# Optimization experiments

Hardware: AMD Instinct MI355X
Metric: run time of the kernel (lower is better)

## Reference

```python
import jax, jax.numpy as jnp
import numpy as np

MAX_N_LATENT = 8
EOS_THRESHOLD = 0.7
EOS_PATTERN_LEN = 3
COS_SIM_THRESHOLD = 0.3
EOS_SOFT_THRESHOLD = 0.5
CONTEXT_WINDOW = 2
EPS = 1e-8


def setup_inputs() -> dict:
    key = jax.random.key(0)
    k = jax.random.split(key, 8)
    B, S, D = 8, 4096, 1024
    s = 0.02
    latent_states = jax.random.normal(k[0], (B, S, D), dtype=jnp.float32)
    binary_mask = jax.random.randint(k[1], (B, S, 1), 0, 2).astype(jnp.int32)
    proj_w = jax.random.normal(k[2], (D, D), dtype=jnp.float32) * s
    proj_b = jax.random.normal(k[3], (D,), dtype=jnp.float32) * s
    eos_w1 = jax.random.normal(k[4], (D, D // 2), dtype=jnp.float32) * s
    eos_b1 = jax.random.normal(k[5], (D // 2,), dtype=jnp.float32) * s
    eos_w2 = jax.random.normal(k[6], (D // 2, 1), dtype=jnp.float32) * s
    eos_b2 = jax.random.normal(k[7], (1,), dtype=jnp.float32) * s
    return {"latent_states": latent_states, "binary_mask": binary_mask,
            "proj_w": proj_w, "proj_b": proj_b,
            "eos_w1": eos_w1, "eos_b1": eos_b1,
            "eos_w2": eos_w2, "eos_b2": eos_b2}


def reference(latent_states, binary_mask, proj_w, proj_b, eos_w1, eos_b1, eos_w2, eos_b2):
    B, S, D = latent_states.shape

    # ---- EOS scores (computed under no_grad in the original) ----
    h = jax.nn.relu(jnp.einsum('bsd,df->bsf', latent_states, eos_w1) + eos_b1)
    eos_scores = jax.nn.sigmoid(jnp.einsum('bsf,fo->bso', h, eos_w2) + eos_b2)[..., 0]
    eos_scores = jax.lax.stop_gradient(eos_scores)  # [B, S]

    # ---- segment ids: a boundary (mask==1) at i closes the patch that includes i ----
    m = binary_mask[..., 0].astype(jnp.int32)                 # [B, S]
    seg = jnp.cumsum(m, axis=1) - m                           # exclusive cumsum => patch id per token
    valid = (seg < MAX_N_LATENT).astype(latent_states.dtype)  # drop patches beyond MAX_N_LATENT (p[:max_patches])
    onehot = jax.nn.one_hot(jnp.clip(seg, 0, MAX_N_LATENT - 1), MAX_N_LATENT,
                            dtype=latent_states.dtype) * valid[..., None]  # [B, S, P]
    sums = jnp.einsum('bsp,bsd->bpd', onehot, latent_states)  # segmented sum
    counts = onehot.sum(axis=1)                               # [B, P]
    pooled = sums / jnp.maximum(counts, 1.0)[..., None]       # mean pooling; empty patches -> 0 (proj adds bias, as in torch)
    patches = jnp.einsum('bpd,do->bpo', pooled, proj_w) + proj_b  # [B, MAX_N_LATENT, output_dim]

    # ---- EOS bounds ----
    mthr = eos_scores > EOS_THRESHOLD
    run = mthr
    for t in range(1, EOS_PATTERN_LEN):                       # consecutive_eos_count >= EOS_PATTERN_LEN
        run = run & jnp.pad(mthr[:, :-t], ((0, 0), (t, 0)))
    a = latent_states[:, 1:-1]                                # prev state at i-1, for i >= 2
    b = latent_states[:, 2:]                                  # current state at i
    cos = (a * b).sum(-1) / (jnp.maximum(jnp.linalg.norm(a, axis=-1), EPS)
                             * jnp.maximum(jnp.linalg.norm(b, axis=-1), EPS))
    cos_rule = jnp.pad((cos < COS_SIM_THRESHOLD) & (eos_scores[:, 2:] > EOS_SOFT_THRESHOLD),
                       ((0, 0), (2, 0)))
    eos_any = run | cos_rule                                  # [B, S] (duplicate triggers don't change min/max)
    has = eos_any.any()
    idx = jnp.arange(S)[None, :]
    first = jnp.min(jnp.where(eos_any, idx, S))
    last = jnp.max(jnp.where(eos_any, idx, -1))
    start = jnp.maximum(0, first - CONTEXT_WINDOW)
    end = jnp.minimum(S - 1, last + CONTEXT_WINDOW)
    eos_bounds = jnp.where(has, jnp.stack([start, end]), jnp.full((2,), -1))
    return patches, eos_bounds
```

## Files before the change

### kernel.cpp

```cpp
#include <hip/hip_runtime.h>
#include <hip/hip_fp16.h>
#include <cstdint>
#include <cstddef>

#define B_ 8
#define S_ 4096
#define D_ 1024
#define H_ 512
#define M_ (B_*S_)

typedef __attribute__((ext_vector_type(8))) _Float16 half8;
typedef __attribute__((ext_vector_type(4))) float f4;

union HU { int4 v; half8 h; };

__device__ inline unsigned short f2h(float f){
  _Float16 h = (_Float16)f;
  return __builtin_bit_cast(unsigned short, h);
}

__global__ void k_init(float* zb, int n, int* fl){
  int i = blockIdx.x*blockDim.x + threadIdx.x;
  for (; i < n; i += gridDim.x*blockDim.x) zb[i] = 0.f;
  if (blockIdx.x==0 && threadIdx.x==0){ fl[0] = 0x7FFFFFFF; fl[1] = -1; }
}

__global__ void k_w1t(const float* __restrict__ w1, unsigned short* __restrict__ w1t){
  __shared__ float tile[32][33];
  int n0 = blockIdx.x*32, k0 = blockIdx.y*32;
  int tx = threadIdx.x, ty = threadIdx.y;
  #pragma unroll
  for (int i=0;i<4;i++) tile[ty+8*i][tx] = w1[(size_t)(k0+ty+8*i)*H_ + n0+tx];
  __syncthreads();
  #pragma unroll
  for (int i=0;i<4;i++) w1t[(size_t)(n0+ty+8*i)*D_ + k0+tx] = f2h(tile[tx][ty+8*i]);
}

__global__ void k_normdot(const float* __restrict__ X, float* __restrict__ n2o,
                          float* __restrict__ dto, unsigned short* __restrict__ Xh){
  int wave = threadIdx.x>>6, lane = threadIdx.x&63;
  int g0 = (blockIdx.x*4 + wave)*16;
  const float4* Xv = (const float4*)X;
  ushort4* Xhv = (ushort4*)Xh;
  float4 pv[4];
  if ((g0 & (S_-1)) != 0){
    size_t bb = (size_t)(g0-1)*256;
    #pragma unroll
    for (int q=0;q<4;q++) pv[q] = Xv[bb + q*64 + lane];
  } else {
    #pragma unroll
    for (int q=0;q<4;q++) pv[q] = make_float4(0.f,0.f,0.f,0.f);
  }
  for (int r=0;r<16;r++){
    int g = g0 + r;
    size_t bb = (size_t)g*256;
    float4 cv[4];
    #pragma unroll
    for (int q=0;q<4;q++) cv[q] = Xv[bb + q*64 + lane];
    float n2=0.f, dp=0.f;
    #pragma unroll
    for (int q=0;q<4;q++){
      n2 += cv[q].x*cv[q].x + cv[q].y*cv[q].y + cv[q].z*cv[q].z + cv[q].w*cv[q].w;
      dp += pv[q].x*cv[q].x + pv[q].y*cv[q].y + pv[q].z*cv[q].z + pv[q].w*cv[q].w;
    }
    #pragma unroll
    for (int q=0;q<4;q++){
      ushort4 u;
      u.x = f2h(cv[q].x); u.y = f2h(cv[q].y); u.z = f2h(cv[q].z); u.w = f2h(cv[q].w);
      Xhv[bb + q*64 + lane] = u;
    }
    #pragma unroll
    for (int off=32; off>0; off>>=1){
      n2 += __shfl_down(n2, off);
      dp += __shfl_down(dp, off);
    }
    if (lane==0){
      n2o[g] = n2;
      if ((g & (S_-1)) != 0) dto[g-1] = dp;
    }
    #pragma unroll
    for (int q=0;q<4;q++) pv[q] = cv[q];
  }
}

#define AS1 __attribute__((address_space(1)))
#define AS3 __attribute__((address_space(3)))

__global__ __launch_bounds__(256) void k_mlp(const unsigned short* __restrict__ Xh,
    const unsigned short* __restrict__ W1T, const float* __restrict__ b1,
    const float* __restrict__ w2, float* __restrict__ logit){
  __shared__ __align__(16) unsigned short As[128*32];
  __shared__ __align__(16) unsigned short Bs[128*32];
  int tid = threadIdx.x;
  int wave = tid>>6, lane = tid&63, quad = lane>>4, l15 = lane&15;
  int m0 = blockIdx.x*128, n0 = blockIdx.y*128;
  int wm = (wave>>1)*64, wn = (wave&1)*64;
  f4 acc[4][4] = {};

  const unsigned short* agp0 = Xh  + (size_t)(m0 + wave*32 + (lane>>2))*D_ + (lane&3)*8;
  const unsigned short* agp1 = agp0 + (size_t)16*D_;
  const unsigned short* bgp0 = W1T + (size_t)(n0 + wave*32 + (lane>>2))*D_ + (lane&3)*8;
  const unsigned short* bgp1 = bgp0 + (size_t)16*D_;
  char* al0 = (char*)As + (wave*2+0)*1024;
  char* al1 = (char*)As + (wave*2+1)*1024;
  char* bl0 = (char*)Bs + (wave*2+0)*1024;
  char* bl1 = (char*)Bs + (wave*2+1)*1024;

  for (int kt=0; kt<32; ++kt){
    int k0 = kt*32;
    __builtin_amdgcn_global_load_lds((const AS1 void*)(agp0 + k0), (AS3 void*)al0, 16, 0, 0);
    __builtin_amdgcn_global_load_lds((const AS1 void*)(agp1 + k0), (AS3 void*)al1, 16, 0, 0);
    __builtin_amdgcn_global_load_lds((const AS1 void*)(bgp0 + k0), (AS3 void*)bl0, 16, 0, 0);
    __builtin_amdgcn_global_load_lds((const AS1 void*)(bgp1 + k0), (AS3 void*)bl1, 16, 0, 0);
    __syncthreads();
    HU a[4], b[4];
    const int4* As4 = (const int4*)As;
    const int4* Bs4 = (const int4*)Bs;
    #pragma unroll
    for (int i=0;i<4;i++) a[i].v = As4[(wm + 16*i + l15)*4 + quad];
    #pragma unroll
    for (int j=0;j<4;j++) b[j].v = Bs4[(wn + 16*j + l15)*4 + quad];
    #pragma unroll
    for (int i=0;i<4;i++){
      #pragma unroll
      for (int j=0;j<4;j++){
        acc[i][j] = __builtin_amdgcn_mfma_f32_16x16x32_f16(a[i].h, b[j].h, acc[i][j], 0, 0, 0);
      }
    }
    __syncthreads();
  }

  float b1v[4], w2v[4];
  #pragma unroll
  for (int j=0;j<4;j++){
    int n = n0 + wn + 16*j + l15;
    b1v[j] = b1[n]; w2v[j] = w2[n];
  }
  #pragma unroll
  for (int i=0;i<4;i++){
    #pragma unroll
    for (int reg=0; reg<4; reg++){
      float p = 0.f;
      #pragma unroll
      for (int j=0;j<4;j++){
        float h = acc[i][j][reg] + b1v[j];
        h = fmaxf(h, 0.f);
        p += w2v[j]*h;
      }
      p += __shfl_xor(p, 1);
      p += __shfl_xor(p, 2);
      p += __shfl_xor(p, 4);
      p += __shfl_xor(p, 8);
      if (l15 == 0) atomicAdd(&logit[m0 + wm + 16*i + quad*4 + reg], p);
    }
  }
}

__global__ void k_chunkbase(const int* __restrict__ mask, int* __restrict__ cb){
  __shared__ int sc[256];
  int b = blockIdx.x, t = threadIdx.x;
  const int* mrow = mask + (size_t)b*S_ + t*16;
  int s = 0;
  #pragma unroll
  for (int i=0;i<16;i++) s += mrow[i];
  sc[t] = s;
  __syncthreads();
  for (int off=1; off<256; off<<=1){
    int v = (t>=off) ? sc[t-off] : 0;
    __syncthreads();
    sc[t] += v;
    __syncthreads();
  }
  if ((t & 15) == 0) cb[b*16 + (t>>4)] = (t==0) ? 0 : sc[t-1];
}

__global__ void k_pool(const float* __restrict__ X, const int* __restrict__ mask,
                       const int* __restrict__ cb, float* __restrict__ gsums,
                       float* __restrict__ gcnt){
  int c = blockIdx.x, b = blockIdx.y, tid = threadIdx.x;
  int base = cb[b*16 + c];
  if (base >= 8) return;
  __shared__ float lsum[8*1024];
  __shared__ int seg[256];
  __shared__ float lcnt[8];
  __shared__ int send_s;
  for (int e=tid; e<8192; e+=256) lsum[e] = 0.f;
  if (tid==0){
    float cnts[8] = {0,0,0,0,0,0,0,0};
    const int* mrow = mask + (size_t)b*S_ + c*256;
    int running = base, i = 0;
    for (; i<256; ++i){
      if (running >= 8) break;
      seg[i] = running;
      cnts[running] += 1.f;
      running += mrow[i];
    }
    send_s = i;
    #pragma unroll
    for (int p=0;p<8;p++) lcnt[p] = cnts[p];
  }
  __syncthreads();
  int send = send_s;
  for (int s2=0; s2<send; ++s2){
    int sg = seg[s2];
    size_t gb = ((size_t)(b*S_ + c*256 + s2))*D_;
    #pragma unroll
    for (int q=0;q<4;q++){
      int d = tid + q*256;
      lsum[sg*1024 + d] += X[gb + d];
    }
  }
  __syncthreads();
  for (int e=tid; e<8192; e+=256){
    float v = lsum[e];
    if (v != 0.f) atomicAdd(&gsums[(size_t)b*8192 + e], v);
  }
  if (tid < 8){
    float v = lcnt[tid];
    if (v != 0.f) atomicAdd(&gcnt[b*8 + tid], v);
  }
}

__global__ __launch_bounds__(256) void k_patch(const float* __restrict__ gsums,
                        const float* __restrict__ gcnt,
                        const float* __restrict__ pw, const float* __restrict__ pb,
                        float* __restrict__ out){
  __shared__ float pool[8192];
  __shared__ float red[2048];
  int b = blockIdx.y, cx = blockIdx.x, tid = threadIdx.x;
  const float4* gs4 = (const float4*)(gsums + (size_t)b*8192);
  float4* pool4 = (float4*)pool;
  for (int e4=tid; e4<2048; e4+=256){
    int p = e4>>8;
    float inv = 1.f / fmaxf(gcnt[b*8 + p], 1.f);
    float4 v = gs4[e4];
    v.x*=inv; v.y*=inv; v.z*=inv; v.w*=inv;
    pool4[e4] = v;
  }
  __syncthreads();
  int c = tid & 31, ks = tid >> 5;
  int col = cx*32 + c;
  float acc[8] = {0,0,0,0,0,0,0,0};
  for (int k=ks*128; k<ks*128+128; ++k){
    float w = pw[(size_t)k*D_ + col];
    #pragma unroll
    for (int p=0;p<8;p++) acc[p] += pool[p*1024 + k]*w;
  }
  #pragma unroll
  for (int p=0;p<8;p++) red[tid*8 + p] = acc[p];
  __syncthreads();
  {
    int p = tid>>5, cc = tid&31;
    float s = 0.f;
    #pragma unroll
    for (int k2=0;k2<8;k2++) s += red[(k2*32 + cc)*8 + p];
    out[(size_t)(b*8+p)*D_ + cx*32 + cc] = s + pb[cx*32 + cc];
  }
}

__global__ void k_flags(const float* __restrict__ logit, const float* __restrict__ n2,
                        const float* __restrict__ dt, const float* __restrict__ b2p,
                        int* __restrict__ fl){
  int g = blockIdx.x*256 + threadIdx.x;
  float b2 = b2p[0];
  int s = g & (S_-1);
  bool any = false;
  if (s >= 2){
    float z0 = logit[g] + b2;
    float z1 = logit[g-1] + b2;
    float z2 = logit[g-2] + b2;
    const float THR = 0.8472978603872037f;
    bool run = (z0 > THR) & (z1 > THR) & (z2 > THR);
    float na = fmaxf(sqrtf(n2[g-1]), 1e-8f);
    float nb = fmaxf(sqrtf(n2[g]), 1e-8f);
    bool cosr = (dt[g-1] < 0.3f*na*nb) & (z0 > 0.f);
    any = run | cosr;
  }
  int mn = any ? s : 0x7FFFFFFF;
  int mx = any ? s : -1;
  #pragma unroll
  for (int off=32; off>0; off>>=1){
    mn = min(mn, __shfl_down(mn, off));
    mx = max(mx, __shfl_down(mx, off));
  }
  if ((threadIdx.x & 63) == 0){
    atomicMin(&fl[0], mn);
    atomicMax(&fl[1], mx);
  }
}

__global__ void k_bounds(const int* __restrict__ fl, float* __restrict__ ob){
  int f = fl[0], l = fl[1];
  if (l < 0){ ob[0] = -1.f; ob[1] = -1.f; }
  else {
    int st = f - 2; if (st < 0) st = 0;
    int en = l + 2; if (en > S_-1) en = S_-1;
    ob[0] = (float)st; ob[1] = (float)en;
  }
}

extern "C" void kernel_launch(void* const* d_in, const int* in_sizes, int n_in,
                              void* d_out, int out_size, void* d_ws, size_t ws_size,
                              hipStream_t stream){
  const float* latent = (const float*)d_in[0];
  const int*   mask   = (const int*)d_in[1];
  const float* proj_w = (const float*)d_in[2];
  const float* proj_b = (const float*)d_in[3];
  const float* eos_w1 = (const float*)d_in[4];
  const float* eos_b1 = (const float*)d_in[5];
  const float* eos_w2 = (const float*)d_in[6];
  const float* eos_b2 = (const float*)d_in[7];
  float* out = (float*)d_out;

  char* ws = (char*)d_ws;
  unsigned short* W1T = (unsigned short*)ws;
  unsigned short* Xh  = (unsigned short*)(ws + 1048576);
  float* fbase = (float*)(ws + 1048576 + 67108864);
  float* logit = fbase;
  float* norm2 = fbase + 32768;
  float* dotv  = fbase + 65536;
  float* gsums = fbase + 98304;
  float* gcnt  = fbase + 163840;
  int* chunkbase = (int*)(fbase + 163904);
  int* firstlast = (int*)(fbase + 164032);

  k_init<<<256, 256, 0, stream>>>(fbase, 163904, firstlast);
  k_w1t<<<dim3(16,32), dim3(32,8), 0, stream>>>(eos_w1, W1T);
  k_normdot<<<512, 256, 0, stream>>>(latent, norm2, dotv, Xh);
  k_chunkbase<<<8, 256, 0, stream>>>(mask, chunkbase);
  k_pool<<<dim3(16,8), 256, 0, stream>>>(latent, mask, chunkbase, gsums, gcnt);
  k_patch<<<dim3(32,8), 256, 0, stream>>>(gsums, gcnt, proj_w, proj_b, out);
  k_mlp<<<dim3(256,4), 256, 0, stream>>>(Xh, W1T, eos_b1, eos_w2, logit);
  k_flags<<<128, 256, 0, stream>>>(logit, norm2, dotv, eos_b2, firstlast);
  k_bounds<<<1,1,0,stream>>>(firstlast, out + 65536);
}
```

Measured before the change: 315.8 us.

## Use 32x32x16 MFMA with K=64 swizzled LDS tiles and merge small kernels

```diff
diff --git a/kernel.cpp b/kernel.cpp
--- a/kernel.cpp
+++ b/kernel.cpp
@@ -10,7 +10,7 @@
 #define M_ (B_*S_)
 
 typedef __attribute__((ext_vector_type(8))) _Float16 half8;
-typedef __attribute__((ext_vector_type(4))) float f4;
+typedef __attribute__((ext_vector_type(16))) float f16v;
 
 union HU { int4 v; half8 h; };
 
@@ -19,21 +19,46 @@
   return __builtin_bit_cast(unsigned short, h);
 }
 
-__global__ void k_init(float* zb, int n, int* fl){
-  int i = blockIdx.x*blockDim.x + threadIdx.x;
-  for (; i < n; i += gridDim.x*blockDim.x) zb[i] = 0.f;
-  if (blockIdx.x==0 && threadIdx.x==0){ fl[0] = 0x7FFFFFFF; fl[1] = -1; }
-}
-
-__global__ void k_w1t(const float* __restrict__ w1, unsigned short* __restrict__ w1t){
+__global__ __launch_bounds__(256) void k_prep(const float* __restrict__ w1,
+    unsigned short* __restrict__ w1t, const int* __restrict__ mask,
+    int* __restrict__ cb, float* __restrict__ logit, float* __restrict__ gsums,
+    float* __restrict__ gcnt, int* __restrict__ fl){
   __shared__ float tile[32][33];
-  int n0 = blockIdx.x*32, k0 = blockIdx.y*32;
-  int tx = threadIdx.x, ty = threadIdx.y;
-  #pragma unroll
-  for (int i=0;i<4;i++) tile[ty+8*i][tx] = w1[(size_t)(k0+ty+8*i)*H_ + n0+tx];
-  __syncthreads();
-  #pragma unroll
-  for (int i=0;i<4;i++) w1t[(size_t)(n0+ty+8*i)*D_ + k0+tx] = f2h(tile[tx][ty+8*i]);
+  __shared__ int sc[256];
+  int b = blockIdx.x, tid = threadIdx.x;
+  if (b < 512){
+    int n0 = (b&15)*32, k0 = (b>>4)*32;
+    int tx = tid&31, ty = tid>>5;
+    #pragma unroll
+    for (int i=0;i<4;i++) tile[ty+8*i][tx] = w1[(size_t)(k0+ty+8*i)*H_ + n0+tx];
+    __syncthreads();
+    #pragma unroll
+    for (int i=0;i<4;i++) w1t[(size_t)(n0+ty+8*i)*D_ + k0+tx] = f2h(tile[tx][ty+8*i]);
+  } else {
+    int bb = b - 512;
+    const int* mrow = mask + (size_t)bb*S_ + tid*16;
+    int s = 0;
+    #pragma unroll
+    for (int i=0;i<16;i++) s += mrow[i];
+    sc[tid] = s;
+    __syncthreads();
+    for (int off=1; off<256; off<<=1){
+      int v = (tid>=off) ? sc[tid-off] : 0;
+      __syncthreads();
+      sc[tid] += v;
+      __syncthreads();
+    }
+    if ((tid & 15) == 0) cb[bb*16 + (tid>>4)] = (tid==0) ? 0 : sc[tid-1];
+    float4* lz = (float4*)(logit + bb*4096);
+    #pragma unroll
+    for (int e=tid; e<1024; e+=256) lz[e] = make_float4(0.f,0.f,0.f,0.f);
+    float4* gz = (float4*)(gsums + (size_t)bb*8192);
+    for (int e=tid; e<2048; e+=256) gz[e] = make_float4(0.f,0.f,0.f,0.f);
+    if (bb==0){
+      if (tid < 64) gcnt[tid] = 0.f;
+      if (tid == 64){ fl[0] = 0x7FFFFFFF; fl[1] = -1; fl[2] = 0; }
+    }
+  }
 }
 
 __global__ void k_normdot(const float* __restrict__ X, float* __restrict__ n2o,
@@ -89,89 +114,90 @@
 __global__ __launch_bounds__(256) void k_mlp(const unsigned short* __restrict__ Xh,
     const unsigned short* __restrict__ W1T, const float* __restrict__ b1,
     const float* __restrict__ w2, float* __restrict__ logit){
-  __shared__ __align__(16) unsigned short As[128*32];
-  __shared__ __align__(16) unsigned short Bs[128*32];
+  __shared__ __align__(16) unsigned short As[128*64];
+  __shared__ __align__(16) unsigned short Bs[128*64];
   int tid = threadIdx.x;
-  int wave = tid>>6, lane = tid&63, quad = lane>>4, l15 = lane&15;
+  int wave = tid>>6, lane = tid&63;
+  int l31 = lane&31, h = lane>>5;
   int m0 = blockIdx.x*128, n0 = blockIdx.y*128;
   int wm = (wave>>1)*64, wn = (wave&1)*64;
-  f4 acc[4][4] = {};
-
-  const unsigned short* agp0 = Xh  + (size_t)(m0 + wave*32 + (lane>>2))*D_ + (lane&3)*8;
-  const unsigned short* agp1 = agp0 + (size_t)16*D_;
-  const unsigned short* bgp0 = W1T + (size_t)(n0 + wave*32 + (lane>>2))*D_ + (lane&3)*8;
-  const unsigned short* bgp1 = bgp0 + (size_t)16*D_;
-  char* al0 = (char*)As + (wave*2+0)*1024;
-  char* al1 = (char*)As + (wave*2+1)*1024;
-  char* bl0 = (char*)Bs + (wave*2+0)*1024;
-  char* bl1 = (char*)Bs + (wave*2+1)*1024;
-
-  for (int kt=0; kt<32; ++kt){
-    int k0 = kt*32;
-    __builtin_amdgcn_global_load_lds((const AS1 void*)(agp0 + k0), (AS3 void*)al0, 16, 0, 0);
-    __builtin_amdgcn_global_load_lds((const AS1 void*)(agp1 + k0), (AS3 void*)al1, 16, 0, 0);
-    __builtin_amdgcn_global_load_lds((const AS1 void*)(bgp0 + k0), (AS3 void*)bl0, 16, 0, 0);
-    __builtin_amdgcn_global_load_lds((const AS1 void*)(bgp1 + k0), (AS3 void*)bl1, 16, 0, 0);
+  f16v acc[2][2] = {};
+
+  int arow = lane>>3;
+  int cch  = (lane&7) ^ arow;
+  const unsigned short* agp[4]; const unsigned short* bgp[4];
+  unsigned aldo[4], bldo[4];
+  #pragma unroll
+  for (int q=0;q<4;q++){
+    int rb = wave*32 + q*8;
+    agp[q] = Xh  + (size_t)(m0 + rb + arow)*D_ + cch*8;
+    bgp[q] = W1T + (size_t)(n0 + rb + arow)*D_ + cch*8;
+    aldo[q] = rb*128;
+    bldo[q] = rb*128;
+  }
+
+  unsigned aoff[2][4], boff[2][4];
+  #pragma unroll
+  for (int i=0;i<2;i++){
+    int m = wm + 32*i + l31;
+    int n = wn + 32*i + l31;
+    #pragma unroll
+    for (int kk=0;kk<4;kk++){
+      int c = kk*2 + h;
+      aoff[i][kk] = m*128 + (((c ^ (m&7)))<<4);
+      boff[i][kk] = n*128 + (((c ^ (n&7)))<<4);
+    }
+  }
+
+  for (int kt=0; kt<16; ++kt){
+    int k0e = kt*64;
+    #pragma unroll
+    for (int q=0;q<4;q++)
+      __builtin_amdgcn_global_load_lds((const AS1 void*)(agp[q] + k0e),
+                                       (AS3 void*)((char*)As + aldo[q]), 16, 0, 0);
+    #pragma unroll
+    for (int q=0;q<4;q++)
+      __builtin_amdgcn_global_load_lds((const AS1 void*)(bgp[q] + k0e),
+                                       (AS3 void*)((char*)Bs + bldo[q]), 16, 0, 0);
     __syncthreads();
-    HU a[4], b[4];
-    const int4* As4 = (const int4*)As;
-    const int4* Bs4 = (const int4*)Bs;
-    #pragma unroll
-    for (int i=0;i<4;i++) a[i].v = As4[(wm + 16*i + l15)*4 + quad];
-    #pragma unroll
-    for (int j=0;j<4;j++) b[j].v = Bs4[(wn + 16*j + l15)*4 + quad];
-    #pragma unroll
-    for (int i=0;i<4;i++){
-      #pragma unroll
-      for (int j=0;j<4;j++){
-        acc[i][j] = __builtin_amdgcn_mfma_f32_16x16x32_f16(a[i].h, b[j].h, acc[i][j], 0, 0, 0);
-      }
+    #pragma unroll
+    for (int kk=0;kk<4;kk++){
+      HU a0, a1, b0, b1u;
+      a0.v  = *(const int4*)((const char*)As + aoff[0][kk]);
+      a1.v  = *(const int4*)((const char*)As + aoff[1][kk]);
+      b0.v  = *(const int4*)((const char*)Bs + boff[0][kk]);
+      b1u.v = *(const int4*)((const char*)Bs + boff[1][kk]);
+      acc[0][0] = __builtin_amdgcn_mfma_f32_32x32x16_f16(a0.h, b0.h,  acc[0][0], 0,0,0);
+      acc[0][1] = __builtin_amdgcn_mfma_f32_32x32x16_f16(a0.h, b1u.h, acc[0][1], 0,0,0);
+      acc[1][0] = __builtin_amdgcn_mfma_f32_32x32x16_f16(a1.h, b0.h,  acc[1][0], 0,0,0);
+      acc[1][1] = __builtin_amdgcn_mfma_f32_32x32x16_f16(a1.h, b1u.h, acc[1][1], 0,0,0);
     }
     __syncthreads();
   }
 
-  float b1v[4], w2v[4];
-  #pragma unroll
-  for (int j=0;j<4;j++){
-    int n = n0 + wn + 16*j + l15;
+  float b1v[2], w2v[2];
+  #pragma unroll
+  for (int j=0;j<2;j++){
+    int n = n0 + wn + 32*j + l31;
     b1v[j] = b1[n]; w2v[j] = w2[n];
   }
   #pragma unroll
-  for (int i=0;i<4;i++){
-    #pragma unroll
-    for (int reg=0; reg<4; reg++){
-      float p = 0.f;
-      #pragma unroll
-      for (int j=0;j<4;j++){
-        float h = acc[i][j][reg] + b1v[j];
-        h = fmaxf(h, 0.f);
-        p += w2v[j]*h;
-      }
+  for (int i=0;i<2;i++){
+    #pragma unroll
+    for (int r=0;r<16;r++){
+      float p = w2v[0]*fmaxf(acc[i][0][r] + b1v[0], 0.f)
+              + w2v[1]*fmaxf(acc[i][1][r] + b1v[1], 0.f);
       p += __shfl_xor(p, 1);
       p += __shfl_xor(p, 2);
       p += __shfl_xor(p, 4);
       p += __shfl_xor(p, 8);
-      if (l15 == 0) atomicAdd(&logit[m0 + wm + 16*i + quad*4 + reg], p);
-    }
-  }
-}
-
-__global__ void k_chunkbase(const int* __restrict__ mask, int* __restrict__ cb){
-  __shared__ int sc[256];
-  int b = blockIdx.x, t = threadIdx.x;
-  const int* mrow = mask + (size_t)b*S_ + t*16;
-  int s = 0;
-  #pragma unroll
-  for (int i=0;i<16;i++) s += mrow[i];
-  sc[t] = s;
-  __syncthreads();
-  for (int off=1; off<256; off<<=1){
-    int v = (t>=off) ? sc[t-off] : 0;
-    __syncthreads();
-    sc[t] += v;
-    __syncthreads();
-  }
-  if ((t & 15) == 0) cb[b*16 + (t>>4)] = (t==0) ? 0 : sc[t-1];
+      p += __shfl_xor(p, 16);
+      if (l31 == 0){
+        int row = m0 + wm + 32*i + (r&3) + 8*(r>>2) + 4*h;
+        atomicAdd(&logit[row], p);
+      }
+    }
+  }
 }
 
 __global__ void k_pool(const float* __restrict__ X, const int* __restrict__ mask,
@@ -258,9 +284,9 @@
   }
 }
 
-__global__ void k_flags(const float* __restrict__ logit, const float* __restrict__ n2,
+__global__ void k_flagsb(const float* __restrict__ logit, const float* __restrict__ n2,
                         const float* __restrict__ dt, const float* __restrict__ b2p,
-                        int* __restrict__ fl){
+                        int* __restrict__ fl, float* __restrict__ ob){
   int g = blockIdx.x*256 + threadIdx.x;
   float b2 = b2p[0];
   int s = g & (S_-1);
@@ -287,15 +313,20 @@
     atomicMin(&fl[0], mn);
     atomicMax(&fl[1], mx);
   }
-}
-
-__global__ void k_bounds(const int* __restrict__ fl, float* __restrict__ ob){
-  int f = fl[0], l = fl[1];
-  if (l < 0){ ob[0] = -1.f; ob[1] = -1.f; }
-  else {
-    int st = f - 2; if (st < 0) st = 0;
-    int en = l + 2; if (en > S_-1) en = S_-1;
-    ob[0] = (float)st; ob[1] = (float)en;
+  __syncthreads();
+  if (threadIdx.x == 0){
+    __threadfence();
+    int old = atomicAdd(&fl[2], 1);
+    if (old == gridDim.x - 1){
+      int f = atomicMin(&fl[0], 0x7FFFFFFF);
+      int l = atomicMax(&fl[1], (int)0x80000000);
+      if (l < 0){ ob[0] = -1.f; ob[1] = -1.f; }
+      else {
+        int st = f - 2; if (st < 0) st = 0;
+        int en = l + 2; if (en > S_-1) en = S_-1;
+        ob[0] = (float)st; ob[1] = (float)en;
+      }
+    }
   }
 }
 
@@ -322,15 +353,12 @@
   float* gsums = fbase + 98304;
   float* gcnt  = fbase + 163840;
   int* chunkbase = (int*)(fbase + 163904);
-  int* firstlast = (int*)(fbase + 164032);
-
-  k_init<<<256, 256, 0, stream>>>(fbase, 163904, firstlast);
-  k_w1t<<<dim3(16,32), dim3(32,8), 0, stream>>>(eos_w1, W1T);
+  int* fl        = (int*)(fbase + 164032);
+
+  k_prep<<<520, 256, 0, stream>>>(eos_w1, W1T, mask, chunkbase, logit, gsums, gcnt, fl);
   k_normdot<<<512, 256, 0, stream>>>(latent, norm2, dotv, Xh);
-  k_chunkbase<<<8, 256, 0, stream>>>(mask, chunkbase);
   k_pool<<<dim3(16,8), 256, 0, stream>>>(latent, mask, chunkbase, gsums, gcnt);
   k_patch<<<dim3(32,8), 256, 0, stream>>>(gsums, gcnt, proj_w, proj_b, out);
   k_mlp<<<dim3(256,4), 256, 0, stream>>>(Xh, W1T, eos_b1, eos_w2, logit);
-  k_flags<<<128, 256, 0, stream>>>(logit, norm2, dotv, eos_b2, firstlast);
-  k_bounds<<<1,1,0,stream>>>(firstlast, out + 65536);
-}
+  k_flagsb<<<128, 256, 0, stream>>>(logit, norm2, dotv, eos_b2, fl, out + 65536);
+}
```

Result: no change. 317.5 us (+0.5%).
